# Optimization experiments

Hardware: AMD Instinct MI355X
Metric: run time of the kernel (lower is better)

## Reference

```python
import jax, jax.numpy as jnp
import numpy as np

B, T, I, H, L, O = 128, 1024, 256, 1024, 2, 128


def setup_inputs() -> dict:
    key = jax.random.key(0)
    ks = jax.random.split(key, 11)
    s = 0.02  # small init scale for stable gates
    inp = {
        "x": jax.random.normal(ks[0], (B, T, I), dtype=jnp.float32),
        # PyTorch LSTM params, gate order (i, f, g, o) stacked along 4H
        "w_ih0": jax.random.normal(ks[1], (4 * H, I), dtype=jnp.float32) * s,
        "w_hh0": jax.random.normal(ks[2], (4 * H, H), dtype=jnp.float32) * s,
        "b_ih0": jax.random.normal(ks[3], (4 * H,), dtype=jnp.float32) * s,
        "b_hh0": jax.random.normal(ks[4], (4 * H,), dtype=jnp.float32) * s,
        "w_ih1": jax.random.normal(ks[5], (4 * H, H), dtype=jnp.float32) * s,
        "w_hh1": jax.random.normal(ks[6], (4 * H, H), dtype=jnp.float32) * s,
        "b_ih1": jax.random.normal(ks[7], (4 * H,), dtype=jnp.float32) * s,
        "b_hh1": jax.random.normal(ks[8], (4 * H,), dtype=jnp.float32) * s,
        "w_out": jax.random.normal(ks[9], (O, H), dtype=jnp.float32) * s,
        "b_out": jax.random.normal(ks[10], (O,), dtype=jnp.float32) * s,
    }
    return inp


def _lstm_layer(x, w_ih, w_hh, b_ih, b_hh):
    # x: [B, T, Din] -> ys: [B, T, H], h_T: [B, H]
    # Precompute input-side gate projections for all timesteps (one big GEMM).
    xg = jnp.einsum("bti,gi->btg", x, w_ih) + b_ih + b_hh  # [B, T, 4H]
    h0 = jnp.zeros((x.shape[0], H), dtype=x.dtype)
    c0 = jnp.zeros((x.shape[0], H), dtype=x.dtype)

    def step(carry, xg_t):
        h, c = carry
        gates = xg_t + h @ w_hh.T  # [B, 4H]
        i, f, g, o = jnp.split(gates, 4, axis=-1)
        i = jax.nn.sigmoid(i)
        f = jax.nn.sigmoid(f)
        g = jnp.tanh(g)
        o = jax.nn.sigmoid(o)
        c_new = f * c + i * g
        h_new = o * jnp.tanh(c_new)
        return (h_new, c_new), h_new

    (h_T, _), ys = jax.lax.scan(step, (h0, c0), jnp.swapaxes(xg, 0, 1))
    return jnp.swapaxes(ys, 0, 1), h_T


def reference(x, w_ih0, w_hh0, b_ih0, b_hh0, w_ih1, w_hh1, b_ih1, b_hh1, w_out, b_out):
    y0, _ = _lstm_layer(x, w_ih0, w_hh0, b_ih0, b_hh0)
    _, h_last = _lstm_layer(y0, w_ih1, w_hh1, b_ih1, b_hh1)
    return h_last @ w_out.T + b_out  # [B, O]
```

## Files before the change

### kernel.cpp

```cpp
#include <hip/hip_runtime.h>
#include <hip/hip_bf16.h>

#define B_ 128
#define T_ 1024
#define I_ 256
#define H_ 1024
#define O_ 128
#define NWG 256
#define HS_ 131072

typedef __attribute__((ext_vector_type(4))) float f32x4;
typedef __attribute__((ext_vector_type(8))) short s16x8;

__device__ __forceinline__ unsigned short f2bf(float f){
  union { float f; unsigned int u; } a; a.f = f;
  unsigned int r = a.u + 0x7FFFu + ((a.u >> 16) & 1u);
  return (unsigned short)(r >> 16);
}
__device__ __forceinline__ float sigmf(float x){ return 1.f/(1.f+__expf(-x)); }
__device__ __forceinline__ float tanhf_(float x){ return 2.f/(1.f+__expf(-2.f*x)) - 1.f; }

__device__ __forceinline__ void ld_frag(s16x8 &d, const unsigned short* p){
  asm volatile("global_load_dwordx4 %0, %1, off sc1" : "=v"(d) : "v"(p) : "memory");
}
__device__ __forceinline__ void ld_f4c(f32x4 &d, const float* p){
  asm volatile("global_load_dwordx4 %0, %1, off sc1" : "=v"(d) : "v"(p) : "memory");
}
__device__ __forceinline__ void st_h(unsigned short* p, unsigned short v){
  __hip_atomic_store(p, v, __ATOMIC_RELAXED, __HIP_MEMORY_SCOPE_AGENT);
}
__device__ __forceinline__ void st_f(float* p, float v){
  __hip_atomic_store(p, v, __ATOMIC_RELAXED, __HIP_MEMORY_SCOPE_AGENT);
}

template<int N>
__device__ __forceinline__ void waitpair(s16x8 &x, s16x8 &y){
  if      constexpr (N==14) asm volatile("s_waitcnt vmcnt(14)" : "+v"(x), "+v"(y) :: "memory");
  else if constexpr (N==12) asm volatile("s_waitcnt vmcnt(12)" : "+v"(x), "+v"(y) :: "memory");
  else if constexpr (N==10) asm volatile("s_waitcnt vmcnt(10)" : "+v"(x), "+v"(y) :: "memory");
  else if constexpr (N==8)  asm volatile("s_waitcnt vmcnt(8)"  : "+v"(x), "+v"(y) :: "memory");
  else if constexpr (N==6)  asm volatile("s_waitcnt vmcnt(6)"  : "+v"(x), "+v"(y) :: "memory");
  else if constexpr (N==4)  asm volatile("s_waitcnt vmcnt(4)"  : "+v"(x), "+v"(y) :: "memory");
  else if constexpr (N==2)  asm volatile("s_waitcnt vmcnt(2)"  : "+v"(x), "+v"(y) :: "memory");
  else                      asm volatile("s_waitcnt vmcnt(0)"  : "+v"(x), "+v"(y) :: "memory");
}
__device__ __forceinline__ void vm_drain(){
  asm volatile("s_waitcnt vmcnt(0)" ::: "memory");
}

__device__ __forceinline__ void bar_arrive(unsigned* base, int gwg, int tid){
  vm_drain();
  __syncthreads();
  if (tid == 0)
    __hip_atomic_fetch_add(&base[(gwg & 7) << 6], 1u, __ATOMIC_RELAXED, __HIP_MEMORY_SCOPE_AGENT);
}
__device__ __forceinline__ void bar_wait(unsigned* base, unsigned tgt32, int tid){
  if (tid < 8){
    while (__hip_atomic_load(&base[tid << 6], __ATOMIC_RELAXED, __HIP_MEMORY_SCOPE_AGENT) < tgt32)
      __builtin_amdgcn_s_sleep(2);
  }
  __syncthreads();
}


__global__ void k_cast_x(const float* __restrict__ x, unsigned short* __restrict__ xb, int n4){
  int i = blockIdx.x*blockDim.x + threadIdx.x;
  if (i >= n4) return;
  f32x4 v = reinterpret_cast<const f32x4*>(x)[i];
  ushort4 o;
  o.x = f2bf(v[0]); o.y = f2bf(v[1]); o.z = f2bf(v[2]); o.w = f2bf(v[3]);
  reinterpret_cast<ushort4*>(xb)[i] = o;
}

__global__ void k_prep_w0(const float* __restrict__ wih, const float* __restrict__ whh,
                          unsigned short* __restrict__ out){
  int n = blockIdx.x*256 + threadIdx.x;
  int j = n & 7, r = (n >> 3) & 15;
  int t = n >> 7;
  int kb = t % 160, gw = t / 160;
  int k = kb*8 + j;
  int grow = (r >> 2)*H_ + gw*4 + (r & 3);
  float v = (k < I_) ? wih[grow*I_ + k] : whh[grow*H_ + (k - I_)];
  out[n] = f2bf(v);
}

__global__ void k_prep_w1(const float* __restrict__ wih, const float* __restrict__ whh,
                          unsigned short* __restrict__ out){
  int n = blockIdx.x*256 + threadIdx.x;
  int j = n & 7, r = (n >> 3) & 15;
  int t = n >> 7;
  int kb = t & 255, gw = t >> 8;
  int k = kb*8 + j;
  int grow = (r >> 2)*H_ + gw*4 + (r & 3);
  float v = (k < H_) ? wih[grow*H_ + k] : whh[grow*H_ + (k - H_)];
  out[n] = f2bf(v);
}

__global__ void k_prep_b(const float* __restrict__ bi0, const float* __restrict__ bh0,
                         const float* __restrict__ bi1, const float* __restrict__ bh1,
                         float* __restrict__ b0, float* __restrict__ b1){
  int n = blockIdx.x*256 + threadIdx.x;
  int layer = n >> 12; int rem = n & 4095;
  int gw = rem >> 4, r = rem & 15;
  int grow = (r >> 2)*H_ + gw*4 + (r & 3);
  if (layer == 0) b0[rem] = bi0[grow] + bh0[grow];
  else            b1[rem] = bi1[grow] + bh1[grow];
}


struct KArgs {
  const unsigned short* xb;
  const float* x32;
  const unsigned short* w0l;
  const unsigned short* w1l;
  const float* b0l;
  const float* b1l;
  unsigned short* h0;
  unsigned short* h1;
  float* hfin;
  const float* wout;
  const float* bout;
  float* y;
  unsigned* cnt;
};

__device__ __forceinline__ void epi(f32x4 (&acc)[2], float (&cs)[2][4], float bias,
                                    unsigned short* __restrict__ hw,
                                    float* __restrict__ hfin,
                                    int wv, int lane, int gwg){
  const int u  = lane & 3;
  const int g0 = (lane >> 2) & 3;
  const int bq = lane >> 4;
  const int ug = (gwg << 2) + u;
  const int kc = ug >> 5;
  const int kg = (ug >> 3) & 3;
  const int jj = ug & 7;
  #pragma unroll
  for (int btl = 0; btl < 2; ++btl){
    const int rb = wv*2 + btl;
    #pragma unroll
    for (int r = 0; r < 4; ++r){
      float pre = acc[btl][r] + bias;
      float q1 = __shfl_xor(pre, 4);
      float q2 = __shfl_xor(pre, 8);
      float q3 = __shfl_xor(pre, 12);
      float iv = (g0==0)?pre:((g0==1)?q1:((g0==2)?q2:q3));
      float fv = (g0==1)?pre:((g0==0)?q1:((g0==3)?q2:q3));
      float gv = (g0==2)?pre:((g0==3)?q1:((g0==0)?q2:q3));
      float ov = (g0==3)?pre:((g0==2)?q1:((g0==1)?q2:q3));
      iv = sigmf(iv); fv = sigmf(fv); gv = tanhf_(gv); ov = sigmf(ov);
      float cn = fv*cs[btl][r] + iv*gv;
      cs[btl][r] = cn;
      float h = ov*tanhf_(cn);
      if (g0 == 0){
        int brow = bq*4 + r;
        int eidx = (((rb*32 + kc) << 9) + (kg*16 + brow)*8 + jj);
        st_h(&hw[eidx], f2bf(h));
        if (hfin) st_f(&hfin[(rb*16 + brow)*H_ + ug], h);
      }
    }
  }
}

#define MFMA_(A, Bf, C) __builtin_amdgcn_mfma_f32_16x16x32_bf16(A, Bf, C, 0, 0, 0)

#define FUS(i) { \
  const int s_ = (i) & 7; \
  s16x8 w0n_ = wfc, w1n_; \
  if ((i) + 1 < 32) w0n_ = *(const s16x8*)(sW0 + ((9 + (i)) << 9) + (lane << 3)); \
  w1n_ = *(const s16x8*)(sW1 + (((i) + 1) << 9) + (lane << 3)); \
  waitpair<14>(fr[s_][0], fr[s_][1]); \
  acc0[0] = MFMA_(fr[s_][0], wfc, acc0[0]); \
  acc0[1] = MFMA_(fr[s_][1], wfc, acc0[1]); \
  acc1[0] = MFMA_(fr[s_][0], wf1c, acc1[0]); \
  acc1[1] = MFMA_(fr[s_][1], wf1c, acc1[1]); \
  { const int j_ = (i) + 8; \
    const unsigned short* b_ = (j_ < 32) ? h0r : h1r; \
    const int c_ = j_ & 31; \
    ld_frag(fr[s_][0], b_ + ((rdA + c_) << 9) + l8); \
    ld_frag(fr[s_][1], b_ + ((rdB + c_) << 9) + l8); } \
  wfc = w0n_; wf1c = w1n_; }

#define ST2(j, NW) { \
  const int s_ = (j) & 7; \
  s16x8 w1n_ = wf1c; \
  if ((j) + 1 < 32) w1n_ = *(const s16x8*)(sW1 + ((33 + (j)) << 9) + (lane << 3)); \
  waitpair<NW>(fr[s_][0], fr[s_][1]); \
  acc1[0] = MFMA_(fr[s_][0], wf1c, acc1[0]); \
  acc1[1] = MFMA_(fr[s_][1], wf1c, acc1[1]); \
  if ((j) + 8 < 32){ const int c_ = (j) + 8; \
    ld_frag(fr[s_][0], h1r + ((rdA + c_) << 9) + l8); \
    ld_frag(fr[s_][1], h1r + ((rdB + c_) << 9) + l8); } \
  wf1c = w1n_; }

__global__ void __launch_bounds__(256, 1) k_lstm(KArgs a){
  extern __shared__ char smem[];
  unsigned short* sW0 = (unsigned short*)smem;
  unsigned short* sW1 = (unsigned short*)(smem + 40960);
  float* sB    = (float*)(smem + 106496);

  const int tid  = threadIdx.x;
  const int gwg  = blockIdx.x;
  const int wv   = tid >> 6;
  const int lane = tid & 63;
  const int lrow = lane & 15;
  const int kgrp = lane >> 4;
  const int koff = kgrp << 3;

  {
    const s16x8* s0 = (const s16x8*)a.w0l + gwg*2560;
    s16x8* d0 = (s16x8*)sW0;
    for (int i = tid; i < 2560; i += 256) d0[i] = s0[i];
    const s16x8* s1 = (const s16x8*)a.w1l + gwg*4096;
    s16x8* d1 = (s16x8*)sW1;
    for (int i = tid; i < 4096; i += 256) d1[i] = s1[i];
    if (tid < 16){ sB[tid] = a.b0l[gwg*16 + tid]; sB[16 + tid] = a.b1l[gwg*16 + tid]; }
  }
  __syncthreads();

  const float bias0 = sB[lrow];
  const float bias1 = sB[16 + lrow];
  float c0s[2][4] = {{0,0,0,0},{0,0,0,0}};
  float c1s[2][4] = {{0,0,0,0},{0,0,0,0}};

  const int rdA = (wv*2 + 0) << 5;
  const int rdB = (wv*2 + 1) << 5;
  const int l8  = lane << 3;
  const size_t xoff0 = (size_t)((wv*2 + 0)*16 + lrow)*(T_*I_) + koff;
  const size_t xoff1 = (size_t)((wv*2 + 1)*16 + lrow)*(T_*I_) + koff;
  const f32x4 z = {0.f, 0.f, 0.f, 0.f};

  int m3 = 0, m3p1 = 1, m3p2 = 2;

  for (int p = 0; p <= T_; ++p){
    const unsigned short* __restrict__ h0r = a.h0 + m3p2*HS_;
    const unsigned short* __restrict__ h1r = a.h1 + m3p1*HS_;
    unsigned short* __restrict__ h0w = a.h0 + m3  *HS_;
    unsigned short* __restrict__ h1w = a.h1 + m3p2*HS_;

    f32x4 acc0[2] = {z, z};
    f32x4 acc1[2] = {z, z};
    if (p < T_){
      if (a.xb){
        const unsigned short* xp0 = a.xb + xoff0 + p*I_;
        const unsigned short* xp1 = a.xb + xoff1 + p*I_;
        #pragma unroll
        for (int kc = 0; kc < 8; ++kc){
          s16x8 wf = *(const s16x8*)(sW0 + (kc << 9) + (lane << 3));
          s16x8 a0 = *(const s16x8*)(xp0 + (kc << 5));
          s16x8 a1 = *(const s16x8*)(xp1 + (kc << 5));
          acc0[0] = MFMA_(a0, wf, acc0[0]);
          acc0[1] = MFMA_(a1, wf, acc0[1]);
        }
      } else {
        const float* fx0 = a.x32 + xoff0 + p*I_;
        const float* fx1 = a.x32 + xoff1 + p*I_;
        #pragma unroll
        for (int kc = 0; kc < 8; ++kc){
          s16x8 wf = *(const s16x8*)(sW0 + (kc << 9) + (lane << 3));
          union { s16x8 v; unsigned short us[8]; } t0, t1;
          f32x4 p00 = *(const f32x4*)(fx0 + (kc << 5));
          f32x4 p01 = *(const f32x4*)(fx0 + (kc << 5) + 4);
          f32x4 p10 = *(const f32x4*)(fx1 + (kc << 5));
          f32x4 p11 = *(const f32x4*)(fx1 + (kc << 5) + 4);
          #pragma unroll
          for (int j2 = 0; j2 < 4; ++j2){
            t0.us[j2] = f2bf(p00[j2]); t0.us[4+j2] = f2bf(p01[j2]);
            t1.us[j2] = f2bf(p10[j2]); t1.us[4+j2] = f2bf(p11[j2]);
          }
          acc0[0] = MFMA_(t0.v, wf, acc0[0]);
          acc0[1] = MFMA_(t1.v, wf, acc0[1]);
        }
      }
    }

    if (p > 0) bar_wait(a.cnt, 32u * (unsigned)p, tid);

    vm_drain();
    {
      s16x8 fr[8][2];
      #pragma unroll
      for (int s2 = 0; s2 < 8; ++s2){
        ld_frag(fr[s2][0], h0r + ((rdA + s2) << 9) + l8);
        ld_frag(fr[s2][1], h0r + ((rdB + s2) << 9) + l8);
      }
      s16x8 wfc  = *(const s16x8*)(sW0 + (8 << 9) + (lane << 3));
      s16x8 wf1c = *(const s16x8*)(sW1 + (lane << 3));
      #pragma unroll
      for (int i = 0; i < 32; ++i) FUS(i);
      if (p < T_) epi(acc0, c0s, bias0, h0w, nullptr, wv, lane, gwg);
      #pragma unroll
      for (int j = 0; j < 24; ++j) ST2(j, 14);
      ST2(24,14); ST2(25,12); ST2(26,10); ST2(27,8);
      ST2(28,6);  ST2(29,4);  ST2(30,2);  ST2(31,0);
      if (p > 0) epi(acc1, c1s, bias1, h1w, (p == T_) ? a.hfin : nullptr, wv, lane, gwg);
    }

    bar_arrive(a.cnt, gwg, tid);

    m3 = m3p1; m3p1 = m3p2; m3p2 = (m3p2 == 2) ? 0 : m3p2 + 1;
  }

  bar_wait(a.cnt, 32u * (unsigned)(T_ + 1), tid);

  if (gwg < 64){
    const int b = (gwg >> 3)*16 + (tid >> 4);
    const int o = (gwg & 7)*16 + (tid & 15);
    const float* hb = a.hfin + b*H_;
    const f32x4* wr = (const f32x4*)(a.wout + o*H_);
    float s = a.bout[o];
    for (int g = 0; g < 32; ++g){
      f32x4 t0,t1,t2,t3,t4,t5,t6,t7;
      ld_f4c(t0, hb + g*32 +  0); ld_f4c(t1, hb + g*32 +  4);
      ld_f4c(t2, hb + g*32 +  8); ld_f4c(t3, hb + g*32 + 12);
      ld_f4c(t4, hb + g*32 + 16); ld_f4c(t5, hb + g*32 + 20);
      ld_f4c(t6, hb + g*32 + 24); ld_f4c(t7, hb + g*32 + 28);
      asm volatile("s_waitcnt vmcnt(0)"
        : "+v"(t0),"+v"(t1),"+v"(t2),"+v"(t3),"+v"(t4),"+v"(t5),"+v"(t6),"+v"(t7) :: "memory");
      const f32x4 w0 = wr[g*8+0], w1 = wr[g*8+1], w2 = wr[g*8+2], w3 = wr[g*8+3];
      const f32x4 w4 = wr[g*8+4], w5 = wr[g*8+5], w6 = wr[g*8+6], w7 = wr[g*8+7];
      s += t0[0]*w0[0]+t0[1]*w0[1]+t0[2]*w0[2]+t0[3]*w0[3];
      s += t1[0]*w1[0]+t1[1]*w1[1]+t1[2]*w1[2]+t1[3]*w1[3];
      s += t2[0]*w2[0]+t2[1]*w2[1]+t2[2]*w2[2]+t2[3]*w2[3];
      s += t3[0]*w3[0]+t3[1]*w3[1]+t3[2]*w3[2]+t3[3]*w3[3];
      s += t4[0]*w4[0]+t4[1]*w4[1]+t4[2]*w4[2]+t4[3]*w4[3];
      s += t5[0]*w5[0]+t5[1]*w5[1]+t5[2]*w5[2]+t5[3]*w5[3];
      s += t6[0]*w6[0]+t6[1]*w6[1]+t6[2]*w6[2]+t6[3]*w6[3];
      s += t7[0]*w7[0]+t7[1]*w7[1]+t7[2]*w7[2]+t7[3]*w7[3];
    }
    a.y[b*O_ + o] = s;
  }
}


extern "C" void kernel_launch(void* const* d_in, const int* in_sizes, int n_in,
                              void* d_out, int out_size, void* d_ws, size_t ws_size,
                              hipStream_t stream){
  const float* x    = (const float*)d_in[0];
  const float* wih0 = (const float*)d_in[1];
  const float* whh0 = (const float*)d_in[2];
  const float* bih0 = (const float*)d_in[3];
  const float* bhh0 = (const float*)d_in[4];
  const float* wih1 = (const float*)d_in[5];
  const float* whh1 = (const float*)d_in[6];
  const float* bih1 = (const float*)d_in[7];
  const float* bhh1 = (const float*)d_in[8];
  const float* wout = (const float*)d_in[9];
  const float* bout = (const float*)d_in[10];
  float* y = (float*)d_out;

  char* ws = (char*)d_ws;
  size_t off = 0;
  auto alloc = [&](size_t n){ char* p = ws + off; off += (n + 255) & ~(size_t)255; return p; };

  unsigned* cnt = (unsigned*)alloc(2048);
  unsigned short* w0l = (unsigned short*)alloc((size_t)256*160*16*8*2);
  unsigned short* w1l = (unsigned short*)alloc((size_t)256*256*16*8*2);
  float* b0l  = (float*)alloc(256*16*4);
  float* b1l  = (float*)alloc(256*16*4);
  unsigned short* h0 = (unsigned short*)alloc((size_t)3*HS_*2);
  unsigned short* h1 = (unsigned short*)alloc((size_t)3*HS_*2);
  float* hfin = (float*)alloc((size_t)B_*H_*4);
  unsigned short* xb = nullptr;
  size_t xb_bytes = (size_t)B_*T_*I_*2;
  if (ws_size >= off + xb_bytes + 256) xb = (unsigned short*)alloc(xb_bytes);

  hipMemsetAsync(cnt, 0, 2048, stream);
  hipMemsetAsync(h0, 0, (size_t)3*HS_*2, stream);
  hipMemsetAsync(h1, 0, (size_t)3*HS_*2, stream);

  if (xb) k_cast_x<<<dim3((B_*T_*I_/4 + 255)/256), dim3(256), 0, stream>>>(x, xb, B_*T_*I_/4);
  k_prep_w0<<<dim3(5242880/256), dim3(256), 0, stream>>>(wih0, whh0, w0l);
  k_prep_w1<<<dim3(8388608/256), dim3(256), 0, stream>>>(wih1, whh1, w1l);
  k_prep_b<<<dim3(32), dim3(256), 0, stream>>>(bih0, bhh0, bih1, bhh1, b0l, b1l);

  KArgs args;
  args.xb = xb; args.x32 = x;
  args.w0l = w0l; args.w1l = w1l; args.b0l = b0l; args.b1l = b1l;
  args.h0 = h0; args.h1 = h1; args.hfin = hfin;
  args.wout = wout; args.bout = bout; args.y = y;
  args.cnt = cnt;

  (void)hipFuncSetAttribute((const void*)k_lstm,
                            hipFuncAttributeMaxDynamicSharedMemorySize, 106624);
  void* kp[] = { (void*)&args };
  hipError_t e = hipLaunchCooperativeKernel((void*)k_lstm, dim3(NWG), dim3(256),
                                            kp, 106624, stream);
  if (e != hipSuccess){
    k_lstm<<<dim3(NWG), dim3(256), 106624, stream>>>(args);
  }
}
```

Baseline: 11.46 ms.

## Halve persistent workgroups, each handling two hidden-unit slices with streamed layer-1 weights

```diff
diff --git a/kernel.cpp b/kernel.cpp
--- a/kernel.cpp
+++ b/kernel.cpp
@@ -6,7 +6,7 @@
 #define I_ 256
 #define H_ 1024
 #define O_ 128
-#define NWG 256
+#define NWG 128
 #define HS_ 131072
 
 typedef __attribute__((ext_vector_type(4))) float f32x4;
@@ -23,6 +23,9 @@
 __device__ __forceinline__ void ld_frag(s16x8 &d, const unsigned short* p){
   asm volatile("global_load_dwordx4 %0, %1, off sc1" : "=v"(d) : "v"(p) : "memory");
 }
+__device__ __forceinline__ void ld_w(s16x8 &d, const unsigned short* p){
+  asm volatile("global_load_dwordx4 %0, %1, off" : "=v"(d) : "v"(p) : "memory");
+}
 __device__ __forceinline__ void ld_f4c(f32x4 &d, const float* p){
   asm volatile("global_load_dwordx4 %0, %1, off sc1" : "=v"(d) : "v"(p) : "memory");
 }
@@ -35,7 +38,11 @@
 
 template<int N>
 __device__ __forceinline__ void waitpair(s16x8 &x, s16x8 &y){
-  if      constexpr (N==14) asm volatile("s_waitcnt vmcnt(14)" : "+v"(x), "+v"(y) :: "memory");
+  if      constexpr (N==28) asm volatile("s_waitcnt vmcnt(28)" : "+v"(x), "+v"(y) :: "memory");
+  else if constexpr (N==24) asm volatile("s_waitcnt vmcnt(24)" : "+v"(x), "+v"(y) :: "memory");
+  else if constexpr (N==20) asm volatile("s_waitcnt vmcnt(20)" : "+v"(x), "+v"(y) :: "memory");
+  else if constexpr (N==16) asm volatile("s_waitcnt vmcnt(16)" : "+v"(x), "+v"(y) :: "memory");
+  else if constexpr (N==14) asm volatile("s_waitcnt vmcnt(14)" : "+v"(x), "+v"(y) :: "memory");
   else if constexpr (N==12) asm volatile("s_waitcnt vmcnt(12)" : "+v"(x), "+v"(y) :: "memory");
   else if constexpr (N==10) asm volatile("s_waitcnt vmcnt(10)" : "+v"(x), "+v"(y) :: "memory");
   else if constexpr (N==8)  asm volatile("s_waitcnt vmcnt(8)"  : "+v"(x), "+v"(y) :: "memory");
@@ -54,9 +61,9 @@
   if (tid == 0)
     __hip_atomic_fetch_add(&base[(gwg & 7) << 6], 1u, __ATOMIC_RELAXED, __HIP_MEMORY_SCOPE_AGENT);
 }
-__device__ __forceinline__ void bar_wait(unsigned* base, unsigned tgt32, int tid){
+__device__ __forceinline__ void bar_wait(unsigned* base, unsigned tgt, int tid){
   if (tid < 8){
-    while (__hip_atomic_load(&base[tid << 6], __ATOMIC_RELAXED, __HIP_MEMORY_SCOPE_AGENT) < tgt32)
+    while (__hip_atomic_load(&base[tid << 6], __ATOMIC_RELAXED, __HIP_MEMORY_SCOPE_AGENT) < tgt)
       __builtin_amdgcn_s_sleep(2);
   }
   __syncthreads();
@@ -127,11 +134,11 @@
 __device__ __forceinline__ void epi(f32x4 (&acc)[2], float (&cs)[2][4], float bias,
                                     unsigned short* __restrict__ hw,
                                     float* __restrict__ hfin,
-                                    int wv, int lane, int gwg){
+                                    int wv, int lane, int ub){
   const int u  = lane & 3;
   const int g0 = (lane >> 2) & 3;
   const int bq = lane >> 4;
-  const int ug = (gwg << 2) + u;
+  const int ug = ub + u;
   const int kc = ug >> 5;
   const int kg = (ug >> 3) & 3;
   const int jj = ug & 7;
@@ -166,41 +173,47 @@
 
 #define FUS(i) { \
   const int s_ = (i) & 7; \
-  s16x8 w0n_ = wfc, w1n_; \
-  if ((i) + 1 < 32) w0n_ = *(const s16x8*)(sW0 + ((9 + (i)) << 9) + (lane << 3)); \
-  w1n_ = *(const s16x8*)(sW1 + (((i) + 1) << 9) + (lane << 3)); \
   waitpair<14>(fr[s_][0], fr[s_][1]); \
-  acc0[0] = MFMA_(fr[s_][0], wfc, acc0[0]); \
-  acc0[1] = MFMA_(fr[s_][1], wfc, acc0[1]); \
-  acc1[0] = MFMA_(fr[s_][0], wf1c, acc1[0]); \
-  acc1[1] = MFMA_(fr[s_][1], wf1c, acc1[1]); \
+  s16x8 wL0 = *(const s16x8*)(sW0u + ((8 + (i)) << 9) + l8); \
+  s16x8 wH0 = *(const s16x8*)(sW0u + 20480 + ((8 + (i)) << 9) + l8); \
+  s16x8 wL1 = *(const s16x8*)(sW1u + ((i) << 9) + l8); \
+  s16x8 wH1 = *(const s16x8*)(sW1u + 16384 + ((i) << 9) + l8); \
+  acc0L[0] = MFMA_(fr[s_][0], wL0, acc0L[0]); \
+  acc0L[1] = MFMA_(fr[s_][1], wL0, acc0L[1]); \
+  acc0H[0] = MFMA_(fr[s_][0], wH0, acc0H[0]); \
+  acc0H[1] = MFMA_(fr[s_][1], wH0, acc0H[1]); \
+  acc1L[0] = MFMA_(fr[s_][0], wL1, acc1L[0]); \
+  acc1L[1] = MFMA_(fr[s_][1], wL1, acc1L[1]); \
+  acc1H[0] = MFMA_(fr[s_][0], wH1, acc1H[0]); \
+  acc1H[1] = MFMA_(fr[s_][1], wH1, acc1H[1]); \
   { const int j_ = (i) + 8; \
     const unsigned short* b_ = (j_ < 32) ? h0r : h1r; \
     const int c_ = j_ & 31; \
     ld_frag(fr[s_][0], b_ + ((rdA + c_) << 9) + l8); \
-    ld_frag(fr[s_][1], b_ + ((rdB + c_) << 9) + l8); } \
-  wfc = w0n_; wf1c = w1n_; }
+    ld_frag(fr[s_][1], b_ + ((rdB + c_) << 9) + l8); } }
 
 #define ST2(j, NW) { \
   const int s_ = (j) & 7; \
-  s16x8 w1n_ = wf1c; \
-  if ((j) + 1 < 32) w1n_ = *(const s16x8*)(sW1 + ((33 + (j)) << 9) + (lane << 3)); \
   waitpair<NW>(fr[s_][0], fr[s_][1]); \
-  acc1[0] = MFMA_(fr[s_][0], wf1c, acc1[0]); \
-  acc1[1] = MFMA_(fr[s_][1], wf1c, acc1[1]); \
-  if ((j) + 8 < 32){ const int c_ = (j) + 8; \
+  acc1L[0] = MFMA_(fr[s_][0], wrg[s_][0], acc1L[0]); \
+  acc1L[1] = MFMA_(fr[s_][1], wrg[s_][0], acc1L[1]); \
+  acc1H[0] = MFMA_(fr[s_][0], wrg[s_][1], acc1H[0]); \
+  acc1H[1] = MFMA_(fr[s_][1], wrg[s_][1], acc1H[1]); \
+  if ((j) < 24){ const int c_ = (j) + 8; \
     ld_frag(fr[s_][0], h1r + ((rdA + c_) << 9) + l8); \
-    ld_frag(fr[s_][1], h1r + ((rdB + c_) << 9) + l8); } \
-  wf1c = w1n_; }
+    ld_frag(fr[s_][1], h1r + ((rdB + c_) << 9) + l8); \
+    ld_w(wrg[s_][0], w1gL + ((40 + (j)) << 9) + l8); \
+    ld_w(wrg[s_][1], w1gH + ((40 + (j)) << 9) + l8); } }
 
 __global__ void __launch_bounds__(256, 1) k_lstm(KArgs a){
   extern __shared__ char smem[];
-  unsigned short* sW0 = (unsigned short*)smem;
-  unsigned short* sW1 = (unsigned short*)(smem + 40960);
-  float* sB    = (float*)(smem + 106496);
+  unsigned short* sW0u = (unsigned short*)smem;
+  unsigned short* sW1u = (unsigned short*)(smem + 81920);
+  float* sB = (float*)(smem + 147456);
 
   const int tid  = threadIdx.x;
   const int gwg  = blockIdx.x;
+  const int w    = gwg;
   const int wv   = tid >> 6;
   const int lane = tid & 63;
   const int lrow = lane & 15;
@@ -208,26 +221,39 @@
   const int koff = kgrp << 3;
 
   {
-    const s16x8* s0 = (const s16x8*)a.w0l + gwg*2560;
-    s16x8* d0 = (s16x8*)sW0;
-    for (int i = tid; i < 2560; i += 256) d0[i] = s0[i];
-    const s16x8* s1 = (const s16x8*)a.w1l + gwg*4096;
-    s16x8* d1 = (s16x8*)sW1;
-    for (int i = tid; i < 4096; i += 256) d1[i] = s1[i];
-    if (tid < 16){ sB[tid] = a.b0l[gwg*16 + tid]; sB[16 + tid] = a.b1l[gwg*16 + tid]; }
+    const s16x8* s0 = (const s16x8*)a.w0l + (size_t)(2*w)*2560;
+    s16x8* d0 = (s16x8*)sW0u;
+    for (int i = tid; i < 5120; i += 256) d0[i] = s0[i];
+    const s16x8* s1a = (const s16x8*)a.w1l + (size_t)(2*w)*4096;
+    s16x8* d1 = (s16x8*)sW1u;
+    for (int i = tid; i < 2048; i += 256) d1[i] = s1a[i];
+    const s16x8* s1b = s1a + 4096;
+    for (int i = tid; i < 2048; i += 256) d1[2048 + i] = s1b[i];
+    if (tid < 16){
+      sB[tid]      = a.b0l[(2*w)*16 + tid];
+      sB[16 + tid] = a.b0l[(2*w + 1)*16 + tid];
+      sB[32 + tid] = a.b1l[(2*w)*16 + tid];
+      sB[48 + tid] = a.b1l[(2*w + 1)*16 + tid];
+    }
   }
   __syncthreads();
 
-  const float bias0 = sB[lrow];
-  const float bias1 = sB[16 + lrow];
-  float c0s[2][4] = {{0,0,0,0},{0,0,0,0}};
-  float c1s[2][4] = {{0,0,0,0},{0,0,0,0}};
+  const float b0L = sB[lrow],      b0H = sB[16 + lrow];
+  const float b1L = sB[32 + lrow], b1H = sB[48 + lrow];
+  float c0L[2][4] = {{0,0,0,0},{0,0,0,0}};
+  float c0H[2][4] = {{0,0,0,0},{0,0,0,0}};
+  float c1L[2][4] = {{0,0,0,0},{0,0,0,0}};
+  float c1H[2][4] = {{0,0,0,0},{0,0,0,0}};
 
   const int rdA = (wv*2 + 0) << 5;
   const int rdB = (wv*2 + 1) << 5;
   const int l8  = lane << 3;
   const size_t xoff0 = (size_t)((wv*2 + 0)*16 + lrow)*(T_*I_) + koff;
   const size_t xoff1 = (size_t)((wv*2 + 1)*16 + lrow)*(T_*I_) + koff;
+  const unsigned short* w0gL = a.w0l + (size_t)(2*w)*20480;
+  const unsigned short* w0gH = w0gL + 20480;
+  const unsigned short* w1gL = a.w1l + (size_t)(2*w)*32768;
+  const unsigned short* w1gH = w1gL + 32768;
   const f32x4 z = {0.f, 0.f, 0.f, 0.f};
 
   int m3 = 0, m3p1 = 1, m3p2 = 2;
@@ -238,26 +264,31 @@
     unsigned short* __restrict__ h0w = a.h0 + m3  *HS_;
     unsigned short* __restrict__ h1w = a.h1 + m3p2*HS_;
 
-    f32x4 acc0[2] = {z, z};
-    f32x4 acc1[2] = {z, z};
+    f32x4 acc0L[2] = {z, z}, acc0H[2] = {z, z};
+    f32x4 acc1L[2] = {z, z}, acc1H[2] = {z, z};
+
     if (p < T_){
       if (a.xb){
-        const unsigned short* xp0 = a.xb + xoff0 + p*I_;
-        const unsigned short* xp1 = a.xb + xoff1 + p*I_;
+        const unsigned short* xp0 = a.xb + xoff0 + (size_t)p*I_;
+        const unsigned short* xp1 = a.xb + xoff1 + (size_t)p*I_;
         #pragma unroll
         for (int kc = 0; kc < 8; ++kc){
-          s16x8 wf = *(const s16x8*)(sW0 + (kc << 9) + (lane << 3));
+          s16x8 wfL = *(const s16x8*)(w0gL + (kc << 9) + l8);
+          s16x8 wfH = *(const s16x8*)(w0gH + (kc << 9) + l8);
           s16x8 a0 = *(const s16x8*)(xp0 + (kc << 5));
           s16x8 a1 = *(const s16x8*)(xp1 + (kc << 5));
-          acc0[0] = MFMA_(a0, wf, acc0[0]);
-          acc0[1] = MFMA_(a1, wf, acc0[1]);
+          acc0L[0] = MFMA_(a0, wfL, acc0L[0]);
+          acc0L[1] = MFMA_(a1, wfL, acc0L[1]);
+          acc0H[0] = MFMA_(a0, wfH, acc0H[0]);
+          acc0H[1] = MFMA_(a1, wfH, acc0H[1]);
         }
       } else {
-        const float* fx0 = a.x32 + xoff0 + p*I_;
-        const float* fx1 = a.x32 + xoff1 + p*I_;
+        const float* fx0 = a.x32 + xoff0 + (size_t)p*I_;
+        const float* fx1 = a.x32 + xoff1 + (size_t)p*I_;
         #pragma unroll
         for (int kc = 0; kc < 8; ++kc){
-          s16x8 wf = *(const s16x8*)(sW0 + (kc << 9) + (lane << 3));
+          s16x8 wfL = *(const s16x8*)(w0gL + (kc << 9) + l8);
+          s16x8 wfH = *(const s16x8*)(w0gH + (kc << 9) + l8);
           union { s16x8 v; unsigned short us[8]; } t0, t1;
           f32x4 p00 = *(const f32x4*)(fx0 + (kc << 5));
           f32x4 p01 = *(const f32x4*)(fx0 + (kc << 5) + 4);
@@ -268,32 +299,51 @@
             t0.us[j2] = f2bf(p00[j2]); t0.us[4+j2] = f2bf(p01[j2]);
             t1.us[j2] = f2bf(p10[j2]); t1.us[4+j2] = f2bf(p11[j2]);
           }
-          acc0[0] = MFMA_(t0.v, wf, acc0[0]);
-          acc0[1] = MFMA_(t1.v, wf, acc0[1]);
+          acc0L[0] = MFMA_(t0.v, wfL, acc0L[0]);
+          acc0L[1] = MFMA_(t1.v, wfL, acc0L[1]);
+          acc0H[0] = MFMA_(t0.v, wfH, acc0H[0]);
+          acc0H[1] = MFMA_(t1.v, wfH, acc0H[1]);
         }
       }
     }
 
-    if (p > 0) bar_wait(a.cnt, 32u * (unsigned)p, tid);
+    if (p > 0) bar_wait(a.cnt, 16u * (unsigned)p, tid);
 
     vm_drain();
     {
       s16x8 fr[8][2];
+      s16x8 wrg[8][2];
       #pragma unroll
       for (int s2 = 0; s2 < 8; ++s2){
         ld_frag(fr[s2][0], h0r + ((rdA + s2) << 9) + l8);
         ld_frag(fr[s2][1], h0r + ((rdB + s2) << 9) + l8);
       }
-      s16x8 wfc  = *(const s16x8*)(sW0 + (8 << 9) + (lane << 3));
-      s16x8 wf1c = *(const s16x8*)(sW1 + (lane << 3));
+      FUS(0)  FUS(1)  FUS(2)  FUS(3)  FUS(4)  FUS(5)  FUS(6)  FUS(7)
+      FUS(8)  FUS(9)  FUS(10) FUS(11) FUS(12) FUS(13) FUS(14) FUS(15)
+      FUS(16) FUS(17) FUS(18) FUS(19) FUS(20) FUS(21) FUS(22) FUS(23)
+      FUS(24) FUS(25) FUS(26) FUS(27) FUS(28) FUS(29) FUS(30) FUS(31)
+      if (p < T_){
+        epi(acc0L, c0L, b0L, h0w, nullptr, wv, lane, (w << 3));
+        epi(acc0H, c0H, b0H, h0w, nullptr, wv, lane, (w << 3) + 4);
+      }
       #pragma unroll
-      for (int i = 0; i < 32; ++i) FUS(i);
-      if (p < T_) epi(acc0, c0s, bias0, h0w, nullptr, wv, lane, gwg);
-      #pragma unroll
-      for (int j = 0; j < 24; ++j) ST2(j, 14);
-      ST2(24,14); ST2(25,12); ST2(26,10); ST2(27,8);
-      ST2(28,6);  ST2(29,4);  ST2(30,2);  ST2(31,0);
-      if (p > 0) epi(acc1, c1s, bias1, h1w, (p == T_) ? a.hfin : nullptr, wv, lane, gwg);
+      for (int s2 = 0; s2 < 8; ++s2){
+        ld_w(wrg[s2][0], w1gL + ((32 + s2) << 9) + l8);
+        ld_w(wrg[s2][1], w1gH + ((32 + s2) << 9) + l8);
+      }
+      ST2(0,8)   ST2(1,8)   ST2(2,8)   ST2(3,8)
+      ST2(4,8)   ST2(5,8)   ST2(6,8)   ST2(7,8)
+      ST2(8,28)  ST2(9,28)  ST2(10,28) ST2(11,28)
+      ST2(12,28) ST2(13,28) ST2(14,28) ST2(15,28)
+      ST2(16,28) ST2(17,28) ST2(18,28) ST2(19,28)
+      ST2(20,28) ST2(21,28) ST2(22,28) ST2(23,28)
+      ST2(24,28) ST2(25,24) ST2(26,20) ST2(27,16)
+      ST2(28,12) ST2(29,8)  ST2(30,4)  ST2(31,0)
+      if (p > 0){
+        float* fin = (p == T_) ? a.hfin : nullptr;
+        epi(acc1L, c1L, b1L, h1w, fin, wv, lane, (w << 3));
+        epi(acc1H, c1H, b1H, h1w, fin, wv, lane, (w << 3) + 4);
+      }
     }
 
     bar_arrive(a.cnt, gwg, tid);
@@ -301,7 +351,7 @@
     m3 = m3p1; m3p1 = m3p2; m3p2 = (m3p2 == 2) ? 0 : m3p2 + 1;
   }
 
-  bar_wait(a.cnt, 32u * (unsigned)(T_ + 1), tid);
+  bar_wait(a.cnt, 16u * (unsigned)(T_ + 1), tid);
 
   if (gwg < 64){
     const int b = (gwg >> 3)*16 + (tid >> 4);
@@ -382,11 +432,11 @@
   args.cnt = cnt;
 
   (void)hipFuncSetAttribute((const void*)k_lstm,
-                            hipFuncAttributeMaxDynamicSharedMemorySize, 106624);
+                            hipFuncAttributeMaxDynamicSharedMemorySize, 147712);
   void* kp[] = { (void*)&args };
   hipError_t e = hipLaunchCooperativeKernel((void*)k_lstm, dim3(NWG), dim3(256),
-                                            kp, 106624, stream);
+                                            kp, 147712, stream);
   if (e != hipSuccess){
-    k_lstm<<<dim3(NWG), dim3(256), 106624, stream>>>(args);
-  }
-}
+    k_lstm<<<dim3(NWG), dim3(256), 147712, stream>>>(args);
+  }
+}
```

Measured after the change: 38.41 ms. 3.35x slower.
